# Optimization experiments

Hardware: AMD Instinct MI355X
Metric: run time of the kernel (lower is better)

Reference implementation:

```python
import jax, jax.numpy as jnp
import numpy as np

EPS = 1e-5  # torch BatchNorm1d default eps


def _project(x, w1, gamma, beta, w2):
    # Linear(bias=False) -> BatchNorm1d (train mode: batch stats, biased var) -> ReLU -> Linear(bias=False)
    h = x @ w1                                   # (n, 128)
    mu = jnp.mean(h, axis=0)
    var = jnp.var(h, axis=0)                     # biased, as torch uses for normalization
    h = (h - mu) * jax.lax.rsqrt(var + EPS) * gamma + beta
    h = jax.nn.relu(h)
    return h @ w2                                # (n, 128)


def setup_inputs() -> dict:
    key = jax.random.key(0)
    k1, k2, k3, k4 = jax.random.split(key, 4)
    latent, hidden = 512, 128
    n_x, n_y = 8192, 2048
    return {
        "variations": jax.random.normal(k1, (n_x, latent), dtype=jnp.float32),
        "exemplar": jax.random.normal(k2, (n_y, latent), dtype=jnp.float32),
        "w1": jax.random.normal(k3, (latent, hidden), dtype=jnp.float32) * (1.0 / np.sqrt(latent)),
        "gamma": jnp.ones((hidden,), dtype=jnp.float32),
        "beta": jnp.zeros((hidden,), dtype=jnp.float32),
        "w2": jax.random.normal(k4, (hidden, hidden), dtype=jnp.float32) * (1.0 / np.sqrt(hidden)),
    }


def reference(variations, exemplar, w1, gamma, beta, w2):
    z1 = _project(variations, w1, gamma, beta, w2)   # (n_x, d)
    z2 = _project(exemplar, w1, gamma, beta, w2)     # (n_y, d)
    # avoids the (n_x, n_y, d) broadcast intermediate of the original)
    x2 = jnp.sum(z1 * z1, axis=1)[:, None]           # (n_x, 1)
    y2 = jnp.sum(z2 * z2, axis=1)[None, :]           # (1, n_y)
    return x2 + y2 - 2.0 * (z1 @ z2.T)               # (n_x, n_y)
```

## Files before the change

kernel.cpp:

```cpp
#include <hip/hip_runtime.h>
#include <hip/hip_bf16.h>


#define LAT 512
#define HID 128
#define EPSV 1e-5f

typedef __attribute__((ext_vector_type(8))) short bf16x8;
typedef __attribute__((ext_vector_type(4))) float f32x4;

__device__ __forceinline__ unsigned short f2bf(float x) {
  unsigned int u = __builtin_bit_cast(unsigned int, x);
  return (unsigned short)((u + 0x7fffu + ((u >> 16) & 1u)) >> 16);
}
__device__ __forceinline__ float bf2f(unsigned short h) {
  unsigned int u = ((unsigned int)h) << 16;
  return __builtin_bit_cast(float, u);
}
__device__ __forceinline__ size_t pack4_off(int strip, int f, int l15, int lq) {
  return (size_t)strip * 2048 + (size_t)(f >> 1) * 512 + (size_t)l15 * 32 +
         (size_t)(((f & 1) * 2 + (lq >> 1)) * 8 + (lq & 1) * 4);
}

__global__ __launch_bounds__(256) void k_prep(const float* __restrict__ W1,
                                              const float* __restrict__ W2,
                                              unsigned short* __restrict__ W1P,
                                              unsigned short* __restrict__ W2T) {
  __shared__ float T[64][65];
  const int t = threadIdx.x;
  int bi = blockIdx.x;
  if (bi < 16) {
    const int tk = bi >> 1, tn = bi & 1;
    const int k0 = tk * 64, n0 = tn * 64;
    {
      const int rr = t >> 4, cc = (t & 15) * 4;
#pragma unroll
      for (int i = 0; i < 4; ++i) {
        const int r = rr + i * 16;
        const float4 v = *(const float4*)(W1 + (size_t)(k0 + r) * HID + n0 + cc);
        T[cc + 0][r] = v.x; T[cc + 1][r] = v.y; T[cc + 2][r] = v.z; T[cc + 3][r] = v.w;
      }
    }
    __syncthreads();
    {
      const int nn = t >> 2, q = (t & 3) * 16;
      const int n = n0 + nn;
      const int f = n >> 4, l15 = n & 15;
#pragma unroll
      for (int e8 = 0; e8 < 2; ++e8) {
        const int kq = q + e8 * 8;
        const int kk = k0 + kq;
        const int tf = kk >> 5, lq = (kk >> 3) & 3;
        const size_t off = ((((size_t)f * 16 + tf) * 16 + l15) * 4 + lq) * 8;
        const ushort4 lo = {f2bf(T[nn][kq + 0]), f2bf(T[nn][kq + 1]),
                            f2bf(T[nn][kq + 2]), f2bf(T[nn][kq + 3])};
        const ushort4 hi = {f2bf(T[nn][kq + 4]), f2bf(T[nn][kq + 5]),
                            f2bf(T[nn][kq + 6]), f2bf(T[nn][kq + 7])};
        *(ushort4*)(W1P + off) = lo;
        *(ushort4*)(W1P + off + 4) = hi;
      }
    }
  } else {
    bi -= 16;
    const int tk = bi >> 1, tn = bi & 1;
    const int k0 = tk * 64, n0 = tn * 64;
    {
      const int rr = t >> 4, cc = (t & 15) * 4;
#pragma unroll
      for (int i = 0; i < 4; ++i) {
        const int r = rr + i * 16;
        const float4 v = *(const float4*)(W2 + (size_t)(k0 + r) * HID + n0 + cc);
        T[cc + 0][r] = v.x; T[cc + 1][r] = v.y; T[cc + 2][r] = v.z; T[cc + 3][r] = v.w;
      }
    }
    __syncthreads();
    {
      const int nn = t >> 2, q = (t & 3) * 16;
      unsigned short* dp = W2T + (size_t)(n0 + nn) * HID + k0 + q;
#pragma unroll
      for (int j = 0; j < 4; ++j) {
        ushort4 o = {f2bf(T[nn][q + j * 4 + 0]), f2bf(T[nn][q + j * 4 + 1]),
                     f2bf(T[nn][q + j * 4 + 2]), f2bf(T[nn][q + j * 4 + 3])};
        *(ushort4*)(dp + j * 4) = o;
      }
    }
  }
}

__global__ __launch_bounds__(256, 1) void k_gemm1(
    const float* __restrict__ X1, const float* __restrict__ X2, int nx,
    const unsigned short* __restrict__ W1P, unsigned short* __restrict__ H,
    float* __restrict__ pS, float* __restrict__ pQ) {
  __shared__ float sS[16][HID], sQ[16][HID];
  const int tid = threadIdx.x, wid = tid >> 6, lane = tid & 63;
  const int l15 = lane & 15, lq = lane >> 4;
  const int browBase = (int)blockIdx.x * 64;
  const int row0 = browBase + wid * 16;
  const int strip = row0 >> 4;
  const float* X = (browBase < nx) ? X1 : X2;
  const int xrow = (browBase < nx) ? row0 : row0 - nx;
  const float* xptr = X + (size_t)(xrow + l15) * LAT + lq * 8;
  const unsigned short* wp = W1P + (size_t)l15 * 32 + lq * 8;
  f32x4 acc[8];
#pragma unroll
  for (int f = 0; f < 8; ++f) acc[f] = (f32x4){0.f, 0.f, 0.f, 0.f};

  float4 xa[4], xb4[4];
  bf16x8 ab[4][8];
#pragma unroll
  for (int p = 0; p < 4; ++p) {
    xa[p] = *(const float4*)(xptr + p * 32);
    xb4[p] = *(const float4*)(xptr + p * 32 + 4);
#pragma unroll
    for (int f = 0; f < 8; ++f)
      ab[p][f] = *(const bf16x8*)(wp + (size_t)(f * 16 + p) * 512);
  }
#pragma unroll
  for (int t = 0; t < 16; ++t) {
    const int s = t & 3;
    const float vv[8] = {xa[s].x, xa[s].y, xa[s].z, xa[s].w,
                         xb4[s].x, xb4[s].y, xb4[s].z, xb4[s].w};
    bf16x8 xv;
#pragma unroll
    for (int i = 0; i < 8; ++i) xv[i] = (short)f2bf(vv[i]);
    if (t + 4 < 16) {
      xa[s] = *(const float4*)(xptr + (t + 4) * 32);
      xb4[s] = *(const float4*)(xptr + (t + 4) * 32 + 4);
    }
#pragma unroll
    for (int f = 0; f < 8; ++f) {
      acc[f] = __builtin_amdgcn_mfma_f32_16x16x32_bf16(ab[s][f], xv, acc[f], 0, 0, 0);
      if (t + 4 < 16)
        ab[s][f] = *(const bf16x8*)(wp + (size_t)(f * 16 + t + 4) * 512);
    }
  }
#pragma unroll
  for (int f = 0; f < 8; ++f) {
    ushort4 hz = {f2bf(acc[f][0]), f2bf(acc[f][1]), f2bf(acc[f][2]), f2bf(acc[f][3])};
    *(ushort4*)(H + pack4_off(strip, f, l15, lq)) = hz;
  }
#pragma unroll
  for (int f = 0; f < 8; ++f) {
    f32x4 s = acc[f];
    f32x4 q = acc[f] * acc[f];
#pragma unroll
    for (int r = 0; r < 4; ++r) {
      s[r] += __shfl_xor(s[r], 1, 64);
      q[r] += __shfl_xor(q[r], 1, 64);
      s[r] += __shfl_xor(s[r], 2, 64);
      q[r] += __shfl_xor(q[r], 2, 64);
    }
    if ((l15 & 3) == 0) {
      *(f32x4*)&sS[wid * 4 + (l15 >> 2)][f * 16 + lq * 4] = s;
      *(f32x4*)&sQ[wid * 4 + (l15 >> 2)][f * 16 + lq * 4] = q;
    }
  }
  __syncthreads();
  if (tid < HID) {
    float s = 0.f, q = 0.f;
#pragma unroll
    for (int r = 0; r < 16; ++r) { s += sS[r][tid]; q += sQ[r][tid]; }
    pS[(size_t)blockIdx.x * HID + tid] = s;
    pQ[(size_t)blockIdx.x * HID + tid] = q;
  }
}

__global__ __launch_bounds__(256) void k_gemm2(
    const unsigned short* __restrict__ H,
    const unsigned short* __restrict__ W2T,
    const float* __restrict__ pS, const float* __restrict__ pQ,
    const float* __restrict__ gamma, const float* __restrict__ beta,
    unsigned short* __restrict__ Z, float* __restrict__ nrm,
    int nb1, int nblk, float n1c, float n2c) {
  __shared__ float s_sc[HID], s_sh[HID];
  __shared__ float t0[2][HID], t1[2][HID];
  const int tid = threadIdx.x, wid = tid >> 6, lane = tid & 63;
  const int l15 = lane & 15, lq = lane >> 4, lk8 = lq * 8;
  const bool set1 = (int)blockIdx.x < nb1;
  {
    const int col = tid & 127, half = tid >> 7;
    const int b0 = set1 ? 0 : nb1;
    const int nb = set1 ? nb1 : (nblk - nb1);
    float s = 0.f, q = 0.f;
#pragma unroll 4
    for (int b = half; b < nb; b += 2) {
      s += pS[(size_t)(b0 + b) * HID + col];
      q += pQ[(size_t)(b0 + b) * HID + col];
    }
    t0[half][col] = s;
    t1[half][col] = q;
  }
  __syncthreads();
  if (tid < HID) {
    const float s = t0[0][tid] + t0[1][tid];
    const float q = t1[0][tid] + t1[1][tid];
    const float n = set1 ? n1c : n2c;
    const float mean = s / n;
    const float var = q / n - mean * mean;
    const float rstd = rsqrtf(var + EPSV);
    const float scale = gamma[tid] * rstd;
    s_sc[tid] = scale;
    s_sh[tid] = beta[tid] - mean * scale;
  }
  __syncthreads();
  const int row0 = (int)blockIdx.x * 64 + wid * 16;
  const int strip = row0 >> 4;
  const unsigned short* hptr = H + (size_t)strip * 2048 + (size_t)l15 * 32 + lk8;
  f32x4 acc[8];
#pragma unroll
  for (int f = 0; f < 8; ++f) acc[f] = (f32x4){0.f, 0.f, 0.f, 0.f};
#pragma unroll
  for (int s = 0; s < 4; ++s) {
    const int k = s * 32 + lk8;
    const bf16x8 hv = *(const bf16x8*)(hptr + (size_t)s * 512);
    const float4 c0 = *(const float4*)&s_sc[k];
    const float4 c1 = *(const float4*)&s_sc[k + 4];
    const float4 d0 = *(const float4*)&s_sh[k];
    const float4 d1 = *(const float4*)&s_sh[k + 4];
    const float cc[8] = {c0.x, c0.y, c0.z, c0.w, c1.x, c1.y, c1.z, c1.w};
    const float dd[8] = {d0.x, d0.y, d0.z, d0.w, d1.x, d1.y, d1.z, d1.w};
    bf16x8 bfr;
#pragma unroll
    for (int i = 0; i < 8; ++i) {
      const float a = fmaxf(fmaf(bf2f((unsigned short)hv[i]), cc[i], dd[i]), 0.f);
      bfr[i] = (short)f2bf(a);
    }
#pragma unroll
    for (int f = 0; f < 8; ++f) {
      const bf16x8 afr = *(const bf16x8*)(W2T + (size_t)(f * 16 + l15) * HID + k);
      acc[f] = __builtin_amdgcn_mfma_f32_16x16x32_bf16(afr, bfr, acc[f], 0, 0, 0);
    }
  }
  float rn = 0.f;
#pragma unroll
  for (int f = 0; f < 8; ++f) {
    rn += acc[f][0] * acc[f][0] + acc[f][1] * acc[f][1] +
          acc[f][2] * acc[f][2] + acc[f][3] * acc[f][3];
    ushort4 z4 = {f2bf(acc[f][0]), f2bf(acc[f][1]), f2bf(acc[f][2]), f2bf(acc[f][3])};
    *(ushort4*)(Z + pack4_off(strip, f, l15, lq)) = z4;
  }
  rn += __shfl_xor(rn, 16, 64);
  rn += __shfl_xor(rn, 32, 64);
  if (lane < 16) nrm[row0 + l15] = rn;
}

__global__ __launch_bounds__(256) void k_dist(const unsigned short* __restrict__ Z1b,
                                              const unsigned short* __restrict__ Z2b,
                                              const float* __restrict__ n1,
                                              const float* __restrict__ n2,
                                              float* __restrict__ D, int NY, int ntx) {
  const int nwg = (int)gridDim.x;
  const int cpx = nwg >> 3;
  const int bid = (int)blockIdx.x;
  const int wgid = (bid & 7) * cpx + (bid >> 3);
  const int tby = wgid / ntx, tbx = wgid - tby * ntx;

  const int tid = threadIdx.x;
  const int wid = tid >> 6, lane = tid & 63;
  const int wr = wid >> 1, wc = wid & 1;
  const int rowB = tby * 128 + wr * 64;
  const int colB = tbx * 128 + wc * 64;
  const int l15 = lane & 15, lq = lane >> 4;
  const unsigned short* Ap = Z1b + (size_t)(rowB >> 4) * 2048 + (size_t)l15 * 32 + lq * 8;
  const unsigned short* Bp = Z2b + (size_t)(colB >> 4) * 2048 + (size_t)l15 * 32 + lq * 8;
  f32x4 acc[4][4];
#pragma unroll
  for (int i = 0; i < 4; ++i)
#pragma unroll
    for (int j = 0; j < 4; ++j) acc[i][j] = (f32x4){0.f, 0.f, 0.f, 0.f};
#pragma unroll
  for (int s = 0; s < 4; ++s) {
    bf16x8 a[4], b[4];
#pragma unroll
    for (int i = 0; i < 4; ++i) a[i] = *(const bf16x8*)(Ap + (size_t)i * 2048 + (size_t)s * 512);
#pragma unroll
    for (int j = 0; j < 4; ++j) b[j] = *(const bf16x8*)(Bp + (size_t)j * 2048 + (size_t)s * 512);
#pragma unroll
    for (int i = 0; i < 4; ++i)
#pragma unroll
      for (int j = 0; j < 4; ++j)
        acc[i][j] = __builtin_amdgcn_mfma_f32_16x16x32_bf16(b[j], a[i], acc[i][j], 0, 0, 0);
  }
  const int cq = lq * 4;
  float na[4];
#pragma unroll
  for (int i = 0; i < 4; ++i) na[i] = n1[rowB + i * 16 + l15];
#pragma unroll
  for (int j = 0; j < 4; ++j) {
    const float4 nbv = *(const float4*)(n2 + colB + j * 16 + cq);
#pragma unroll
    for (int i = 0; i < 4; ++i) {
      float4 o;
      o.x = na[i] + nbv.x - 2.f * acc[i][j][0];
      o.y = na[i] + nbv.y - 2.f * acc[i][j][1];
      o.z = na[i] + nbv.z - 2.f * acc[i][j][2];
      o.w = na[i] + nbv.w - 2.f * acc[i][j][3];
      *(float4*)(D + (size_t)(rowB + i * 16 + l15) * NY + colB + j * 16 + cq) = o;
    }
  }
}

extern "C" void kernel_launch(void* const* d_in, const int* in_sizes, int n_in,
                              void* d_out, int out_size, void* d_ws, size_t ws_size,
                              hipStream_t stream) {
  const float* variations = (const float*)d_in[0];
  const float* exemplar   = (const float*)d_in[1];
  const float* w1         = (const float*)d_in[2];
  const float* gamma      = (const float*)d_in[3];
  const float* beta       = (const float*)d_in[4];
  const float* w2         = (const float*)d_in[5];
  float* D = (float*)d_out;

  const int nx = in_sizes[0] / LAT;
  const int ny = in_sizes[1] / LAT;
  const int nrows = nx + ny;
  const int nbb = nrows / 64;
  const int nb1 = nx / 64;

  char* p = (char*)d_ws;
  unsigned short* Hb  = (unsigned short*)p; p += (size_t)nrows * HID * 2;
  unsigned short* Zb  = (unsigned short*)p; p += (size_t)nrows * HID * 2;
  unsigned short* W1P = (unsigned short*)p; p += (size_t)LAT * HID * 2;
  unsigned short* W2T = (unsigned short*)p; p += (size_t)HID * HID * 2;
  float* pS = (float*)p;  p += (size_t)nbb * HID * 4;
  float* pQ = (float*)p;  p += (size_t)nbb * HID * 4;
  float* nrmAll = (float*)p; p += (size_t)nrows * 4;
  float* n1v = nrmAll;
  float* n2v = nrmAll + nx;
  unsigned short* Z1b = Zb;
  unsigned short* Z2b = Zb + (size_t)nx * HID;

  k_prep<<<20, 256, 0, stream>>>(w1, w2, W1P, W2T);
  k_gemm1<<<nbb, 256, 0, stream>>>(variations, exemplar, nx, W1P, Hb, pS, pQ);
  k_gemm2<<<nbb, 256, 0, stream>>>(Hb, W2T, pS, pQ, gamma, beta, Zb, nrmAll,
                                   nb1, nbb, (float)nx, (float)ny);
  const int ntx = ny / 128;
  const int nwg = (nx / 128) * ntx;
  k_dist<<<nwg, 256, 0, stream>>>(Z1b, Z2b, n1v, n2v, D, ny, ntx);
}
```

Before: 57.29 us.

## Split gemm1 into single-wave blocks per 16-row strip, drop LDS reduction

k_gemm1 now launches one 64-thread wave per 16-row strip instead of four waves per 64-row block. The column partial sums are reduced entirely with wave shuffles and written straight to global memory, which removes the shared-memory staging and the __syncthreads. This gives four times as many blocks, so the scheduler has more freedom and no block waits on a barrier. In exchange, k_gemm2 must read four times as many partial-stat rows when it finalizes the batch-norm statistics.

```diff
diff --git a/kernel.cpp b/kernel.cpp
--- a/kernel.cpp
+++ b/kernel.cpp
@@ -87,18 +87,17 @@
   }
 }
 
-__global__ __launch_bounds__(256, 1) void k_gemm1(
+__global__ __launch_bounds__(64, 1) void k_gemm1(
     const float* __restrict__ X1, const float* __restrict__ X2, int nx,
     const unsigned short* __restrict__ W1P, unsigned short* __restrict__ H,
     float* __restrict__ pS, float* __restrict__ pQ) {
-  __shared__ float sS[16][HID], sQ[16][HID];
-  const int tid = threadIdx.x, wid = tid >> 6, lane = tid & 63;
+  const int lane = threadIdx.x;
   const int l15 = lane & 15, lq = lane >> 4;
-  const int browBase = (int)blockIdx.x * 64;
-  const int row0 = browBase + wid * 16;
-  const int strip = row0 >> 4;
-  const float* X = (browBase < nx) ? X1 : X2;
-  const int xrow = (browBase < nx) ? row0 : row0 - nx;
+  const int strip = (int)blockIdx.x;
+  const int row0 = strip * 16;
+  const bool set1 = row0 < nx;
+  const float* X = set1 ? X1 : X2;
+  const int xrow = set1 ? row0 : row0 - nx;
   const float* xptr = X + (size_t)(xrow + l15) * LAT + lq * 8;
   const unsigned short* wp = W1P + (size_t)l15 * 32 + lq * 8;
   f32x4 acc[8];
@@ -145,23 +144,16 @@
     f32x4 q = acc[f] * acc[f];
 #pragma unroll
     for (int r = 0; r < 4; ++r) {
-      s[r] += __shfl_xor(s[r], 1, 64);
-      q[r] += __shfl_xor(q[r], 1, 64);
-      s[r] += __shfl_xor(s[r], 2, 64);
-      q[r] += __shfl_xor(q[r], 2, 64);
-    }
-    if ((l15 & 3) == 0) {
-      *(f32x4*)&sS[wid * 4 + (l15 >> 2)][f * 16 + lq * 4] = s;
-      *(f32x4*)&sQ[wid * 4 + (l15 >> 2)][f * 16 + lq * 4] = q;
-    }
-  }
-  __syncthreads();
-  if (tid < HID) {
-    float s = 0.f, q = 0.f;
-#pragma unroll
-    for (int r = 0; r < 16; ++r) { s += sS[r][tid]; q += sQ[r][tid]; }
-    pS[(size_t)blockIdx.x * HID + tid] = s;
-    pQ[(size_t)blockIdx.x * HID + tid] = q;
+#pragma unroll
+      for (int m = 1; m <= 8; m <<= 1) {
+        s[r] += __shfl_xor(s[r], m, 64);
+        q[r] += __shfl_xor(q[r], m, 64);
+      }
+    }
+    if (l15 == 0) {
+      *(f32x4*)(pS + (size_t)strip * HID + f * 16 + lq * 4) = s;
+      *(f32x4*)(pQ + (size_t)strip * HID + f * 16 + lq * 4) = q;
+    }
   }
 }
 
@@ -171,16 +163,16 @@
     const float* __restrict__ pS, const float* __restrict__ pQ,
     const float* __restrict__ gamma, const float* __restrict__ beta,
     unsigned short* __restrict__ Z, float* __restrict__ nrm,
-    int nb1, int nblk, float n1c, float n2c) {
+    int pb1, int pnblk, float n1c, float n2c, int nx) {
   __shared__ float s_sc[HID], s_sh[HID];
   __shared__ float t0[2][HID], t1[2][HID];
   const int tid = threadIdx.x, wid = tid >> 6, lane = tid & 63;
   const int l15 = lane & 15, lq = lane >> 4, lk8 = lq * 8;
-  const bool set1 = (int)blockIdx.x < nb1;
+  const bool set1 = ((int)blockIdx.x * 64) < nx;
   {
     const int col = tid & 127, half = tid >> 7;
-    const int b0 = set1 ? 0 : nb1;
-    const int nb = set1 ? nb1 : (nblk - nb1);
+    const int b0 = set1 ? 0 : pb1;
+    const int nb = set1 ? pb1 : (pnblk - pb1);
     float s = 0.f, q = 0.f;
 #pragma unroll 4
     for (int b = half; b < nb; b += 2) {
@@ -314,16 +306,17 @@
   const int nx = in_sizes[0] / LAT;
   const int ny = in_sizes[1] / LAT;
   const int nrows = nx + ny;
+  const int nst = nrows / 16;
+  const int pb1 = nx / 16;
   const int nbb = nrows / 64;
-  const int nb1 = nx / 64;
 
   char* p = (char*)d_ws;
   unsigned short* Hb  = (unsigned short*)p; p += (size_t)nrows * HID * 2;
   unsigned short* Zb  = (unsigned short*)p; p += (size_t)nrows * HID * 2;
   unsigned short* W1P = (unsigned short*)p; p += (size_t)LAT * HID * 2;
   unsigned short* W2T = (unsigned short*)p; p += (size_t)HID * HID * 2;
-  float* pS = (float*)p;  p += (size_t)nbb * HID * 4;
-  float* pQ = (float*)p;  p += (size_t)nbb * HID * 4;
+  float* pS = (float*)p;  p += (size_t)nst * HID * 4;
+  float* pQ = (float*)p;  p += (size_t)nst * HID * 4;
   float* nrmAll = (float*)p; p += (size_t)nrows * 4;
   float* n1v = nrmAll;
   float* n2v = nrmAll + nx;
@@ -331,9 +324,9 @@
   unsigned short* Z2b = Zb + (size_t)nx * HID;
 
   k_prep<<<20, 256, 0, stream>>>(w1, w2, W1P, W2T);
-  k_gemm1<<<nbb, 256, 0, stream>>>(variations, exemplar, nx, W1P, Hb, pS, pQ);
+  k_gemm1<<<nst, 64, 0, stream>>>(variations, exemplar, nx, W1P, Hb, pS, pQ);
   k_gemm2<<<nbb, 256, 0, stream>>>(Hb, W2T, pS, pQ, gamma, beta, Zb, nrmAll,
-                                   nb1, nbb, (float)nx, (float)ny);
+                                   pb1, nst, (float)nx, (float)ny, nx);
   const int ntx = ny / 128;
   const int nwg = (nx / 128) * ntx;
   k_dist<<<nwg, 256, 0, stream>>>(Z1b, Z2b, n1v, n2v, D, ny, ntx);
```

Measured after the change: 70.23 us. 22.6% more time.
